# Kernel optimization log

Measured on AMD Instinct MI355X. Metric: run time of the kernel, lower is better.

Reference implementation:

```python
import jax, jax.numpy as jnp
import numpy as np

# graph sizes: G graphs of N_PER nodes each (block-diagonal batched graph)
G, N_PER, F, NHID, E_PER = 128, 512, 128, 128, 4096
N = G * N_PER
E = G * E_PER
L1, L2, L3 = 4, 2, 2            # PANConv filter sizes (conv1 uses init filter_size=4)
K1, K2, K3 = N_PER // 2, N_PER // 4, N_PER // 8  # ratio=0.5 top-k per pooling stage


def setup_inputs() -> dict:
    ks = jax.random.split(jax.random.key(0), 10)
    rng = np.random.default_rng(0)
    off = (np.arange(G) * N_PER)[:, None]
    src = (rng.integers(0, N_PER, size=(G, E_PER)) + off).reshape(-1)
    dst = (rng.integers(0, N_PER, size=(G, E_PER)) + off).reshape(-1)
    edge_index = jnp.asarray(np.stack([src, dst]).astype(np.int32))
    batch = jnp.repeat(jnp.arange(G, dtype=jnp.int32), N_PER)
    def w(k, shp, fan):
        return jax.random.normal(k, shp, jnp.float32) / np.float32(np.sqrt(fan))
    z = lambda *s: jnp.zeros(s, jnp.float32)
    return dict(
        x=jax.random.normal(ks[0], (N, F), jnp.float32),
        edge_index=edge_index, batch=batch,
        lump_W=w(ks[1], (F, NHID), F), lump_b=z(NHID),
        conv1_W=w(ks[2], (NHID, NHID), NHID), conv1_b=z(NHID),
        conv2_W=w(ks[3], (NHID, NHID), NHID), conv2_b=z(NHID),
        conv3_W=w(ks[4], (NHID, NHID), NHID), conv3_b=z(NHID),
        pool1_p=w(ks[5], (NHID,), NHID), pool1_beta=jnp.full((2,), 0.5, jnp.float32),
        pool2_p=w(ks[6], (NHID,), NHID), pool2_beta=jnp.full((2,), 0.5, jnp.float32),
        pool3_p=w(ks[7], (NHID,), NHID), pool3_beta=jnp.full((2,), 0.5, jnp.float32),
        lin1_W=w(ks[8], (NHID, NHID // 2), NHID), lin1_b=z(NHID // 2),
        lin2_W=w(ks[9], (NHID // 2, 1), NHID // 2), lin2_b=z(1),
    )


def _pan_prop(h, src, dst, ew, L):
    # (sum_{l=0..L} A^l) @ h, A weighted by edge weights ew, via iterated gather/scatter
    acc, y = h, h
    n = h.shape[0]
    for _ in range(L):
        y = jax.ops.segment_sum(y[src] * ew[:, None], dst, num_segments=n)
        acc = acc + y
    return acc


def _pan_conv(x, src, dst, ew, W, b, L):
    # PANConv: M = Z^{-1/2} (sum_{l<=L} A^l) Z^{-1/2};  out = M x W + b
    d = _pan_prop(jnp.ones((x.shape[0], 1), x.dtype), src, dst, ew, L)[:, 0]
    dinv = jax.lax.rsqrt(jnp.maximum(d, 1e-12))
    h = dinv[:, None] * _pan_prop(dinv[:, None] * x, src, dst, ew, L)
    return h @ W + b


def _pan_pool(x, src, dst, ew, p, beta, n_per, k):
    # PANPooling: score = beta0*(x.p)/||p|| + beta1*node_strength; per-graph top-k
    n = x.shape[0]
    deg = jax.ops.segment_sum(ew, dst, num_segments=n)
    score = beta[0] * (x @ p) / jnp.linalg.norm(p) + beta[1] * deg
    _, idx = jax.lax.top_k(score.reshape(G, n_per), k)          # [G, k] local indices
    perm = (idx + (jnp.arange(G) * n_per)[:, None]).reshape(-1)  # [G*k] global
    x_new = x[perm] * jnp.tanh(score[perm])[:, None]
    inv = jnp.zeros((n,), jnp.int32).at[perm].set(jnp.arange(G * k, dtype=jnp.int32))
    mask = jnp.zeros((n,), x.dtype).at[perm].set(1.0)
    # keep edge arrays fixed-size: dropped edges get weight 0 (same math as filtering)
    return x_new, inv[src], inv[dst], ew * mask[src] * mask[dst], perm


def reference(x, edge_index, batch, lump_W, lump_b, conv1_W, conv1_b, conv2_W, conv2_b,
              conv3_W, conv3_b, pool1_p, pool1_beta, pool2_p, pool2_beta, pool3_p,
              pool3_beta, lin1_W, lin1_b, lin2_W, lin2_b):
    src, dst = edge_index[0], edge_index[1]
    ew = jnp.ones((src.shape[0],), x.dtype)
    h = x @ lump_W + lump_b                                   # PANLump lift
    h = _pan_conv(h, src, dst, ew, conv1_W, conv1_b, L1)
    h, src, dst, ew, perm1 = _pan_pool(h, src, dst, ew, pool1_p, pool1_beta, N_PER, K1)
    h = _pan_conv(h, src, dst, ew, conv2_W, conv2_b, L2)
    h, src, dst, ew, perm2 = _pan_pool(h, src, dst, ew, pool2_p, pool2_beta, K1, K2)
    h = _pan_conv(h, src, dst, ew, conv3_W, conv3_b, L3)
    h, src, dst, ew, perm3 = _pan_pool(h, src, dst, ew, pool3_p, pool3_beta, K2, K3)
    seg = jnp.repeat(jnp.arange(G, dtype=jnp.int32), K3)
    mean = jax.ops.segment_sum(h, seg, num_segments=G) / jnp.float32(K3)  # scatter_mean
    out = jax.nn.relu(mean @ lin1_W + lin1_b) @ lin2_W + lin2_b           # [G, 1]
    return out
```

## Files before the change

### kernel.cpp

```cpp
#include <hip/hip_runtime.h>
#include <math.h>

#define G_     128
#define E_     524288
#define EPG    4096
#define DEGMAX 48

typedef __attribute__((ext_vector_type(8))) short bf16x8;
typedef __attribute__((ext_vector_type(4))) float f32x4;
typedef __attribute__((ext_vector_type(4))) unsigned short u16x4;

__device__ inline void split_bf16(float x, short& hi, short& lo){
    unsigned u = __float_as_uint(x);
    hi = (short)(u >> 16);
    float hf = __uint_as_float(u & 0xffff0000u);
    unsigned r = __float_as_uint(x - hf);
    lo = (short)(r >> 16);
}

__global__ __launch_bounds__(512) void k_prep1(const int* __restrict__ ei,
        int* __restrict__ cnt, unsigned short* __restrict__ csrcp,
        int* __restrict__ permg, float* __restrict__ dinvg){
    __shared__ int   lcnt[512];
    __shared__ float y[1024];
    __shared__ int   bins[64];
    __shared__ int   permS[512];
    int g = blockIdx.x, t = threadIdx.x, gbase = g*512;
    lcnt[t] = 0;
    if (t < 64) bins[t] = 0;
    __syncthreads();
    for (int i = t; i < EPG; i += 512){
        int e = g*EPG + i;
        int sv = ei[e] & 511;
        int d  = ei[E_ + e] & 511;
        int slot = atomicAdd(&lcnt[d], 1);
        if (slot < DEGMAX) csrcp[(size_t)(gbase + d)*DEGMAX + slot] = (unsigned short)sv;
    }
    __syncthreads();
    int rawc = lcnt[t];
    cnt[gbase + t] = rawc;
    int dc = min(rawc, DEGMAX);
    atomicAdd(&bins[dc], 1);
    __syncthreads();
    if (t < 64){
        int v0 = bins[t], s = v0;
        #pragma unroll
        for (int off = 1; off < 64; off <<= 1){
            int n = __shfl_up(s, off);
            if (t >= off) s += n;
        }
        bins[t] = s - v0;
    }
    __syncthreads();
    {
        int slot = atomicAdd(&bins[dc], 1);
        int pk = t | (dc << 16);
        permS[slot] = pk;
        permg[gbase + slot] = pk;
    }
    __syncthreads();
    int pk = permS[t];
    int pv = pk & 0xffff, pd = pk >> 16;
    y[pv] = 1.f;
    __syncthreads();
    float dacc = 1.f;
    int cur = 0;
    for (int l = 0; l < 4; l++){
        const float* la = &y[cur*512];
        float s = 0.f;
        int nq = (pd + 3) >> 2;
        const u16x4* cp = (const u16x4*)(csrcp + (size_t)(gbase + pv)*DEGMAX);
        u16x4 oc = cp[0];
        #pragma unroll 1
        for (int jq = 0; jq < nq; jq++){
            u16x4 ocn = cp[jq + 1];
            s += (la[(int)oc[0]] + la[(int)oc[1]]) + (la[(int)oc[2]] + la[(int)oc[3]]);
            oc = ocn;
        }
        if (nq) s -= (float)(nq*4 - pd) * la[0];
        y[(1^cur)*512 + pv] = s;
        dacc += s;
        __syncthreads();
        cur ^= 1;
    }
    dinvg[gbase + pv] = rsqrtf(fmaxf(dacc, 1e-12f));
}

template<int NPER, int L, int IT>
__global__ __launch_bounds__(1024)
void k_prop(const int* __restrict__ permg, const float* __restrict__ dinvg,
        const unsigned short* __restrict__ csrcp,
        const float* __restrict__ X, float* __restrict__ OUT){
    __shared__ __align__(16) float y[NPER*32];
    __shared__ float dinvs[NPER];
    int g = blockIdx.x, fq = blockIdx.y, gbase = g*NPER;
    int t = threadIdx.x;
    int f4 = (t & 7)*4;
    int fo = fq*32 + f4;
    if (t < NPER) dinvs[t] = dinvg[gbase + t];
    int pkr[IT];
    {
        int wv = t >> 6, gi = (t >> 3) & 7;
        #pragma unroll
        for (int it = 0; it < IT; it++){
            int ch = (it & 1) ? (15 - wv) : wv;
            pkr[it] = permg[gbase + (16*it + ch)*8 + gi];
        }
    }
    __syncthreads();
    float4 acc[IT];
    #pragma unroll
    for (int it = 0; it < IT; it++){
        int v = pkr[it] & 0xffff;
        float d = dinvs[v];
        float4 w = *(const float4*)&X[(size_t)(gbase + v)*128 + fo];
        w.x*=d; w.y*=d; w.z*=d; w.w*=d;
        acc[it] = w;
        *(float4*)&y[v*32 + f4] = w;
    }
    __syncthreads();
    for (int l = 0; l < L; l++){
        float4 s[IT];
        #pragma unroll
        for (int it = 0; it < IT; it++){
            int pk = pkr[it];
            int c = pk >> 16;
            int nq = (c + 3) >> 2;
            const u16x4* cp = (const u16x4*)(csrcp + (size_t)(gbase + (pk & 0xffff))*DEGMAX);
            float4 ss = make_float4(0.f,0.f,0.f,0.f);
            u16x4 oc = cp[0];
            #pragma unroll 1
            for (int jq = 0; jq < nq; jq++){
                u16x4 ocn = cp[jq + 1];
                float4 w0 = *(const float4*)&y[((int)oc[0])*32 + f4];
                float4 w1 = *(const float4*)&y[((int)oc[1])*32 + f4];
                float4 w2 = *(const float4*)&y[((int)oc[2])*32 + f4];
                float4 w3 = *(const float4*)&y[((int)oc[3])*32 + f4];
                ss.x += (w0.x + w1.x) + (w2.x + w3.x);
                ss.y += (w0.y + w1.y) + (w2.y + w3.y);
                ss.z += (w0.z + w1.z) + (w2.z + w3.z);
                ss.w += (w0.w + w1.w) + (w2.w + w3.w);
                oc = ocn;
            }
            if (nq){
                float fp = (float)(nq*4 - c);
                float4 z = *(const float4*)&y[f4];
                ss.x -= fp*z.x; ss.y -= fp*z.y; ss.z -= fp*z.z; ss.w -= fp*z.w;
            }
            s[it] = ss;
        }
        __syncthreads();
        #pragma unroll
        for (int it = 0; it < IT; it++){
            int v = pkr[it] & 0xffff;
            *(float4*)&y[v*32 + f4] = s[it];
            acc[it].x+=s[it].x; acc[it].y+=s[it].y; acc[it].z+=s[it].z; acc[it].w+=s[it].w;
        }
        __syncthreads();
    }
    #pragma unroll
    for (int it = 0; it < IT; it++){
        int v = pkr[it] & 0xffff;
        float d = dinvs[v];
        float4 w = acc[it];
        w.x*=d; w.y*=d; w.z*=d; w.w*=d;
        *(float4*)&OUT[(size_t)(gbase + v)*128 + fo] = w;
    }
}

template<int RT>
__global__ __launch_bounds__(256) void k_gemm_mfma(const float* __restrict__ X,
        const float* __restrict__ W, const float* __restrict__ bias, float* __restrict__ Y){
    __shared__ short wsh[128*136];
    __shared__ short wsl[128*136];
    __shared__ float bsh[128];
    int t = threadIdx.x;
    for (int e = t; e < 16384; e += 256){
        int k = e >> 7, n = e & 127;
        short hi, lo; split_bf16(W[e], hi, lo);
        wsh[n*136 + k] = hi; wsl[n*136 + k] = lo;
    }
    if (t < 128) bsh[t] = bias[t];
    __syncthreads();
    int wave = t >> 6, lane = t & 63;
    int ln = lane & 15, q = lane >> 4;
    size_t rb0 = (size_t)blockIdx.x * (64*RT);
    for (int rt = 0; rt < RT; rt++){
        size_t rb = rb0 + (size_t)rt*64;
        const float* xrow = &X[(rb + wave*16 + ln)*128 + q*8];
        f32x4 acc[8];
        #pragma unroll
        for (int i = 0; i < 8; i++) acc[i] = (f32x4){0.f,0.f,0.f,0.f};
        #pragma unroll
        for (int kc = 0; kc < 4; kc++){
            float4 xa = *(const float4*)(xrow + kc*32);
            float4 xb = *(const float4*)(xrow + kc*32 + 4);
            bf16x8 ah, al; short hi, lo;
            split_bf16(xa.x, hi, lo); ah[0]=hi; al[0]=lo;
            split_bf16(xa.y, hi, lo); ah[1]=hi; al[1]=lo;
            split_bf16(xa.z, hi, lo); ah[2]=hi; al[2]=lo;
            split_bf16(xa.w, hi, lo); ah[3]=hi; al[3]=lo;
            split_bf16(xb.x, hi, lo); ah[4]=hi; al[4]=lo;
            split_bf16(xb.y, hi, lo); ah[5]=hi; al[5]=lo;
            split_bf16(xb.z, hi, lo); ah[6]=hi; al[6]=lo;
            split_bf16(xb.w, hi, lo); ah[7]=hi; al[7]=lo;
            #pragma unroll
            for (int nt = 0; nt < 8; nt++){
                int wo = (nt*16 + ln)*136 + kc*32 + q*8;
                bf16x8 bh = *(const bf16x8*)&wsh[wo];
                bf16x8 bl = *(const bf16x8*)&wsl[wo];
                acc[nt] = __builtin_amdgcn_mfma_f32_16x16x32_bf16(ah, bh, acc[nt], 0, 0, 0);
                acc[nt] = __builtin_amdgcn_mfma_f32_16x16x32_bf16(ah, bl, acc[nt], 0, 0, 0);
                acc[nt] = __builtin_amdgcn_mfma_f32_16x16x32_bf16(al, bh, acc[nt], 0, 0, 0);
            }
        }
        #pragma unroll
        for (int nt = 0; nt < 8; nt++){
            int c = nt*16 + ln;
            float bb = bsh[c];
            #pragma unroll
            for (int r = 0; r < 4; r++){
                Y[(rb + wave*16 + q*4 + r)*128 + c] = acc[nt][r] + bb;
            }
        }
    }
}

template<int NPER, bool BUILD>
__global__ __launch_bounds__(512) void k_pooltop(const float* __restrict__ h, const float* __restrict__ p,
        const float* __restrict__ beta, const int* __restrict__ cnt,
        const int* __restrict__ esrc_in, const int* __restrict__ edst_in,
        int* __restrict__ esrc_out, int* __restrict__ edst_out,
        int* __restrict__ cnt_next, unsigned short* __restrict__ csrcp,
        int* __restrict__ permg, float* __restrict__ dinvg,
        float* __restrict__ hout){
    __shared__ __align__(16) float q[128];
    __shared__ __align__(16) float sc[NPER];
    __shared__ float th[NPER];
    __shared__ int  nid[NPER];
    __shared__ float red[64];
    __shared__ int  lcnt[NPER/2];
    __shared__ int  bins[64];
    __shared__ int  permS[NPER/2];
    const int K = NPER/2;
    int g = blockIdx.x, t = threadIdx.x, gbase = g*NPER;
    float b0 = beta[0], b1 = beta[1];
    if (BUILD && t < K) lcnt[t] = 0;
    if (t < 64) bins[t] = 0;
    if (t < 64){ float a = p[t], b = p[t+64]; red[t] = a*a + b*b; }
    __syncthreads();
    if (t == 0){ float s = 0.f; for (int i = 0; i < 64; i++) s += red[i]; red[0] = sqrtf(s); }
    __syncthreads();
    if (t < 128) q[t] = b0 * p[t] / red[0];
    __syncthreads();
    if (t < NPER){
        const float4* hr = (const float4*)(h + (size_t)(gbase + t)*128);
        const float4* q4 = (const float4*)q;
        float s = 0.f;
        #pragma unroll 8
        for (int j = 0; j < 32; j++){
            float4 a = hr[j], b = q4[j];
            s += a.x*b.x + a.y*b.y + a.z*b.z + a.w*b.w;
        }
        s += b1 * (float)cnt[gbase + t];
        sc[t] = s;
    }
    __syncthreads();
    if (t < NPER){
        float s = sc[t];
        int rank = 0;
        const float4* sc4 = (const float4*)sc;
        #pragma unroll 8
        for (int j4 = 0; j4 < NPER/4; j4++){
            float4 v = sc4[j4];
            int j = j4*4;
            rank += (v.x > s) || (v.x == s && (j+0) < t);
            rank += (v.y > s) || (v.y == s && (j+1) < t);
            rank += (v.z > s) || (v.z == s && (j+2) < t);
            rank += (v.w > s) || (v.w == s && (j+3) < t);
        }
        nid[t] = (rank < K) ? (g*K + rank) : -1;
        th[t] = tanhf(s);
    }
    __syncthreads();
    for (int base = t; base < NPER*32; base += 512){
        int v = base >> 5, f4 = base & 31;
        int ni = nid[v];
        if (ni >= 0){
            float tt = th[v];
            float4 w = *(const float4*)&h[(size_t)(gbase + v)*128 + f4*4];
            w.x*=tt; w.y*=tt; w.z*=tt; w.w*=tt;
            *(float4*)&hout[(size_t)ni*128 + f4*4] = w;
        }
    }
    if (BUILD){
        for (int i = t; i < EPG; i += 512){
            int e = g*EPG + i;
            int d = edst_in[e];
            if (d < 0) continue;
            int s_ = esrc_in[e];
            int ns = nid[s_ - gbase], nd = nid[d - gbase];
            if ((ns | nd) < 0){ edst_out[e] = -1; }
            else {
                esrc_out[e] = ns; edst_out[e] = nd;
                int slot = atomicAdd(&lcnt[nd & (K-1)], 1);
                if (slot < DEGMAX) csrcp[(size_t)nd*DEGMAX + slot] = (unsigned short)(ns & (K-1));
            }
        }
        __syncthreads();
        float* yd = sc;
        int rawc = 0, dc = 0;
        if (t < K){
            rawc = lcnt[t];
            cnt_next[g*K + t] = rawc;
            dc = min(rawc, DEGMAX);
            atomicAdd(&bins[dc], 1);
        }
        __syncthreads();
        if (t < 64){
            int v0 = bins[t], s = v0;
            #pragma unroll
            for (int off = 1; off < 64; off <<= 1){
                int n = __shfl_up(s, off);
                if (t >= off) s += n;
            }
            bins[t] = s - v0;
        }
        __syncthreads();
        if (t < K){
            int slot = atomicAdd(&bins[dc], 1);
            permS[slot] = t | (dc << 16);
            permg[g*K + slot] = permS[slot];
        }
        __syncthreads();
        int pv = 0, pd = 0;
        if (t < K){
            int pk = permS[t];
            pv = pk & 0xffff; pd = pk >> 16;
            yd[pv] = 1.f;
        }
        __syncthreads();
        float dacc = 1.f;
        int cur = 0;
        for (int l = 0; l < 2; l++){
            if (t < K){
                const float* la = &yd[cur*K];
                float s = 0.f;
                int nq = (pd + 3) >> 2;
                const u16x4* cp = (const u16x4*)(csrcp + (size_t)(g*K + pv)*DEGMAX);
                u16x4 oc = cp[0];
                #pragma unroll 1
                for (int jq = 0; jq < nq; jq++){
                    u16x4 ocn = cp[jq + 1];
                    s += (la[(int)oc[0]] + la[(int)oc[1]]) + (la[(int)oc[2]] + la[(int)oc[3]]);
                    oc = ocn;
                }
                if (nq) s -= (float)(nq*4 - pd) * la[0];
                yd[(1^cur)*K + pv] = s;
                dacc += s;
            }
            __syncthreads();
            cur ^= 1;
        }
        if (t < K) dinvg[g*K + pv] = rsqrtf(fmaxf(dacc, 1e-12f));
    }
}

__global__ __launch_bounds__(128) void k_meanmlp(const float* __restrict__ h, const float* __restrict__ W1,
        const float* __restrict__ b1, const float* __restrict__ W2, const float* __restrict__ b2,
        float* __restrict__ out){
    __shared__ float mr[128];
    int g = blockIdx.x, t = threadIdx.x;
    float s = 0.f;
    #pragma unroll 8
    for (int r = 0; r < 64; r++) s += h[((size_t)g*64 + r)*128 + t];
    mr[t] = s * (1.f/64.f);
    __syncthreads();
    if (t < 64){
        float a = b1[t];
        #pragma unroll 8
        for (int k = 0; k < 128; k++) a += mr[k]*W1[k*64 + t];
        a = fmaxf(a, 0.f);
        float r = a * W2[t];
        #pragma unroll
        for (int off = 32; off > 0; off >>= 1) r += __shfl_down(r, off);
        if (t == 0) out[g] = r + b2[0];
    }
}

extern "C" void kernel_launch(void* const* d_in, const int* in_sizes, int n_in,
                              void* d_out, int out_size, void* d_ws, size_t ws_size,
                              hipStream_t stream){
    (void)in_sizes; (void)n_in; (void)out_size; (void)ws_size;
    const float* x     = (const float*)d_in[0];
    const int*   ei    = (const int*)d_in[1];
    const float* lumpW = (const float*)d_in[3];
    const float* lumpb = (const float*)d_in[4];
    const float* convW[3]    = {(const float*)d_in[5], (const float*)d_in[7], (const float*)d_in[9]};
    const float* convB[3]    = {(const float*)d_in[6], (const float*)d_in[8], (const float*)d_in[10]};
    const float* poolP[3]    = {(const float*)d_in[11], (const float*)d_in[13], (const float*)d_in[15]};
    const float* poolBeta[3] = {(const float*)d_in[12], (const float*)d_in[14], (const float*)d_in[16]};
    const float* lin1W = (const float*)d_in[17];
    const float* lin1b = (const float*)d_in[18];
    const float* lin2W = (const float*)d_in[19];
    const float* lin2b = (const float*)d_in[20];
    float* out = (float*)d_out;

    char* w8 = (char*)d_ws;
    size_t off = 0;
    auto alloc = [&](size_t bytes)->char*{
        char* p = w8 + off; off += (bytes + 255) & ~(size_t)255; return p;
    };
    float* A     = (float*)alloc((size_t)65536*128*4);
    float* Bb    = (float*)alloc((size_t)65536*128*4);
    float* Cc    = (float*)alloc((size_t)32768*128*4);
    int*   srcA  = (int*)alloc((size_t)E_*4);
    int*   dstA  = (int*)alloc((size_t)E_*4);
    unsigned short* csr1 = (unsigned short*)alloc((size_t)65536*DEGMAX*2);
    unsigned short* csr2 = (unsigned short*)alloc((size_t)32768*DEGMAX*2);
    unsigned short* csr3 = (unsigned short*)alloc((size_t)16384*DEGMAX*2);
    int*   cntA  = (int*)alloc((size_t)(65536+32768+16384)*4);
    int*   cnt1 = cntA, *cnt2 = cntA + 65536, *cnt3 = cntA + 98304;
    int*   perm1 = (int*)alloc((size_t)65536*4);
    int*   perm2 = (int*)alloc((size_t)32768*4);
    int*   perm3 = (int*)alloc((size_t)16384*4);
    float* dinv1 = (float*)alloc((size_t)65536*4);
    float* dinv2 = (float*)alloc((size_t)32768*4);
    float* dinv3 = (float*)alloc((size_t)16384*4);

    dim3 b256(256);

    size_t zbytes = (size_t)(65536+32768+16384)*DEGMAX*2;
    hipMemsetAsync(csr1, 0, zbytes, stream);
    k_gemm_mfma<2><<<512, b256, 0, stream>>>(x, lumpW, lumpb, A);
    k_prep1<<<G_, 512, 0, stream>>>(ei, cnt1, csr1, perm1, dinv1);

    k_prop<512,4,4><<<dim3(G_,4), 1024, 0, stream>>>(perm1, dinv1, csr1, A, Bb);
    k_gemm_mfma<2><<<512, b256, 0, stream>>>(Bb, convW[0], convB[0], A);
    k_pooltop<512,true><<<G_, 512, 0, stream>>>(A, poolP[0], poolBeta[0], cnt1,
            ei, ei + E_, srcA, dstA, cnt2, csr2, perm2, dinv2, Cc);

    k_prop<256,2,2><<<dim3(G_,4), 1024, 0, stream>>>(perm2, dinv2, csr2, Cc, Bb);
    k_gemm_mfma<1><<<512, b256, 0, stream>>>(Bb, convW[1], convB[1], A);
    k_pooltop<256,true><<<G_, 512, 0, stream>>>(A, poolP[1], poolBeta[1], cnt2,
            srcA, dstA, srcA, dstA, cnt3, csr3, perm3, dinv3, Cc);

    k_prop<128,2,1><<<dim3(G_,4), 1024, 0, stream>>>(perm3, dinv3, csr3, Cc, Bb);
    k_gemm_mfma<1><<<256, b256, 0, stream>>>(Bb, convW[2], convB[2], A);
    k_pooltop<128,false><<<G_, 512, 0, stream>>>(A, poolP[2], poolBeta[2], cnt3,
            nullptr, nullptr, nullptr, nullptr, nullptr, nullptr, nullptr, nullptr, Cc);

    k_meanmlp<<<G_, 128, 0, stream>>>(Cc, lin1W, lin1b, lin2W, lin2b, out);
}
```

Baseline: 341.6 us.

## Fuse pool score into GEMM epilogue and gather selected rows lazily

Computes the pooling score (projection onto normalized p plus beta1 times degree) inside the GEMM epilogue, using shuffle reductions over the accumulator tiles. The top-k kernel no longer reads the full feature matrix or writes a compacted, tanh-scaled copy. It emits selected row indices and tanh factors instead, and the next propagation and mean-MLP kernels gather rows through those indices and apply the scale. This removes a full read and write of the feature matrix per pooling stage, at the cost of indirect row gathers in the consumers.

```diff
diff --git a/kernel.cpp b/kernel.cpp
--- a/kernel.cpp
+++ b/kernel.cpp
@@ -86,11 +86,12 @@
     dinvg[gbase + pv] = rsqrtf(fmaxf(dacc, 1e-12f));
 }
 
-template<int NPER, int L, int IT>
+template<int NPER, int L, int IT, bool SEL>
 __global__ __launch_bounds__(1024)
 void k_prop(const int* __restrict__ permg, const float* __restrict__ dinvg,
         const unsigned short* __restrict__ csrcp,
-        const float* __restrict__ X, float* __restrict__ OUT){
+        const float* __restrict__ X, const int* __restrict__ selg,
+        const float* __restrict__ thg, float* __restrict__ OUT){
     __shared__ __align__(16) float y[NPER*32];
     __shared__ float dinvs[NPER];
     int g = blockIdx.x, fq = blockIdx.y, gbase = g*NPER;
@@ -113,7 +114,14 @@
     for (int it = 0; it < IT; it++){
         int v = pkr[it] & 0xffff;
         float d = dinvs[v];
-        float4 w = *(const float4*)&X[(size_t)(gbase + v)*128 + fo];
+        size_t row;
+        if (SEL){
+            row = (size_t)selg[gbase + v];
+            d *= thg[gbase + v];
+        } else {
+            row = (size_t)(gbase + v);
+        }
+        float4 w = *(const float4*)&X[row*128 + fo];
         w.x*=d; w.y*=d; w.z*=d; w.w*=d;
         acc[it] = w;
         *(float4*)&y[v*32 + f4] = w;
@@ -170,10 +178,14 @@
 
 template<int RT>
 __global__ __launch_bounds__(256) void k_gemm_mfma(const float* __restrict__ X,
-        const float* __restrict__ W, const float* __restrict__ bias, float* __restrict__ Y){
+        const float* __restrict__ W, const float* __restrict__ bias, float* __restrict__ Y,
+        const float* __restrict__ p, const float* __restrict__ beta,
+        const int* __restrict__ cntv, float* __restrict__ score){
     __shared__ short wsh[128*136];
     __shared__ short wsl[128*136];
     __shared__ float bsh[128];
+    __shared__ float qs[128];
+    __shared__ float rednorm[64];
     int t = threadIdx.x;
     for (int e = t; e < 16384; e += 256){
         int k = e >> 7, n = e & 127;
@@ -181,7 +193,16 @@
         wsh[n*136 + k] = hi; wsl[n*136 + k] = lo;
     }
     if (t < 128) bsh[t] = bias[t];
-    __syncthreads();
+    if (score && t < 64){ float a = p[t], b = p[t+64]; rednorm[t] = a*a + b*b; }
+    __syncthreads();
+    float b1 = 0.f;
+    if (score){
+        if (t == 0){ float s = 0.f; for (int i = 0; i < 64; i++) s += rednorm[i]; rednorm[0] = sqrtf(s); }
+        __syncthreads();
+        if (t < 128) qs[t] = beta[0] * p[t] / rednorm[0];
+        b1 = beta[1];
+        __syncthreads();
+    }
     int wave = t >> 6, lane = t & 63;
     int ln = lane & 15, q = lane >> 4;
     size_t rb0 = (size_t)blockIdx.x * (64*RT);
@@ -223,48 +244,45 @@
                 Y[(rb + wave*16 + q*4 + r)*128 + c] = acc[nt][r] + bb;
             }
         }
+        if (score){
+            #pragma unroll
+            for (int r = 0; r < 4; r++){
+                float sp = 0.f;
+                #pragma unroll
+                for (int nt = 0; nt < 8; nt++){
+                    int c = nt*16 + ln;
+                    sp += (acc[nt][r] + bsh[c]) * qs[c];
+                }
+                sp += __shfl_xor(sp, 1);
+                sp += __shfl_xor(sp, 2);
+                sp += __shfl_xor(sp, 4);
+                sp += __shfl_xor(sp, 8);
+                if (ln == 0){
+                    int row = (int)rb + wave*16 + q*4 + r;
+                    score[row] = sp + b1 * (float)cntv[row];
+                }
+            }
+        }
     }
 }
 
 template<int NPER, bool BUILD>
-__global__ __launch_bounds__(512) void k_pooltop(const float* __restrict__ h, const float* __restrict__ p,
-        const float* __restrict__ beta, const int* __restrict__ cnt,
+__global__ __launch_bounds__(512) void k_pooltop(const float* __restrict__ score_in,
         const int* __restrict__ esrc_in, const int* __restrict__ edst_in,
         int* __restrict__ esrc_out, int* __restrict__ edst_out,
         int* __restrict__ cnt_next, unsigned short* __restrict__ csrcp,
         int* __restrict__ permg, float* __restrict__ dinvg,
-        float* __restrict__ hout){
-    __shared__ __align__(16) float q[128];
+        int* __restrict__ selg, float* __restrict__ thg){
     __shared__ __align__(16) float sc[NPER];
-    __shared__ float th[NPER];
     __shared__ int  nid[NPER];
-    __shared__ float red[64];
     __shared__ int  lcnt[NPER/2];
     __shared__ int  bins[64];
     __shared__ int  permS[NPER/2];
     const int K = NPER/2;
     int g = blockIdx.x, t = threadIdx.x, gbase = g*NPER;
-    float b0 = beta[0], b1 = beta[1];
     if (BUILD && t < K) lcnt[t] = 0;
     if (t < 64) bins[t] = 0;
-    if (t < 64){ float a = p[t], b = p[t+64]; red[t] = a*a + b*b; }
-    __syncthreads();
-    if (t == 0){ float s = 0.f; for (int i = 0; i < 64; i++) s += red[i]; red[0] = sqrtf(s); }
-    __syncthreads();
-    if (t < 128) q[t] = b0 * p[t] / red[0];
-    __syncthreads();
-    if (t < NPER){
-        const float4* hr = (const float4*)(h + (size_t)(gbase + t)*128);
-        const float4* q4 = (const float4*)q;
-        float s = 0.f;
-        #pragma unroll 8
-        for (int j = 0; j < 32; j++){
-            float4 a = hr[j], b = q4[j];
-            s += a.x*b.x + a.y*b.y + a.z*b.z + a.w*b.w;
-        }
-        s += b1 * (float)cnt[gbase + t];
-        sc[t] = s;
-    }
+    if (t < NPER) sc[t] = score_in[gbase + t];
     __syncthreads();
     if (t < NPER){
         float s = sc[t];
@@ -279,20 +297,13 @@
             rank += (v.z > s) || (v.z == s && (j+2) < t);
             rank += (v.w > s) || (v.w == s && (j+3) < t);
         }
-        nid[t] = (rank < K) ? (g*K + rank) : -1;
-        th[t] = tanhf(s);
-    }
-    __syncthreads();
-    for (int base = t; base < NPER*32; base += 512){
-        int v = base >> 5, f4 = base & 31;
-        int ni = nid[v];
-        if (ni >= 0){
-            float tt = th[v];
-            float4 w = *(const float4*)&h[(size_t)(gbase + v)*128 + f4*4];
-            w.x*=tt; w.y*=tt; w.z*=tt; w.w*=tt;
-            *(float4*)&hout[(size_t)ni*128 + f4*4] = w;
-        }
-    }
+        if (rank < K){
+            nid[t] = g*K + rank;
+            selg[g*K + rank] = gbase + t;
+            thg[g*K + rank]  = tanhf(s);
+        } else nid[t] = -1;
+    }
+    __syncthreads();
     if (BUILD){
         for (int i = t; i < EPG; i += 512){
             int e = g*EPG + i;
@@ -366,14 +377,19 @@
     }
 }
 
-__global__ __launch_bounds__(128) void k_meanmlp(const float* __restrict__ h, const float* __restrict__ W1,
-        const float* __restrict__ b1, const float* __restrict__ W2, const float* __restrict__ b2,
+__global__ __launch_bounds__(128) void k_meanmlp(const float* __restrict__ h,
+        const int* __restrict__ selg, const float* __restrict__ thg,
+        const float* __restrict__ W1, const float* __restrict__ b1,
+        const float* __restrict__ W2, const float* __restrict__ b2,
         float* __restrict__ out){
     __shared__ float mr[128];
     int g = blockIdx.x, t = threadIdx.x;
     float s = 0.f;
     #pragma unroll 8
-    for (int r = 0; r < 64; r++) s += h[((size_t)g*64 + r)*128 + t];
+    for (int r = 0; r < 64; r++){
+        int row = selg[g*64 + r];
+        s += h[(size_t)row*128 + t] * thg[g*64 + r];
+    }
     mr[t] = s * (1.f/64.f);
     __syncthreads();
     if (t < 64){
@@ -413,7 +429,6 @@
     };
     float* A     = (float*)alloc((size_t)65536*128*4);
     float* Bb    = (float*)alloc((size_t)65536*128*4);
-    float* Cc    = (float*)alloc((size_t)32768*128*4);
     int*   srcA  = (int*)alloc((size_t)E_*4);
     int*   dstA  = (int*)alloc((size_t)E_*4);
     unsigned short* csr1 = (unsigned short*)alloc((size_t)65536*DEGMAX*2);
@@ -427,28 +442,44 @@
     float* dinv1 = (float*)alloc((size_t)65536*4);
     float* dinv2 = (float*)alloc((size_t)32768*4);
     float* dinv3 = (float*)alloc((size_t)16384*4);
+    float* score1 = (float*)alloc((size_t)65536*4);
+    float* score2 = (float*)alloc((size_t)32768*4);
+    float* score3 = (float*)alloc((size_t)16384*4);
+    int*   sel2  = (int*)alloc((size_t)32768*4);
+    int*   sel3  = (int*)alloc((size_t)16384*4);
+    int*   sel4  = (int*)alloc((size_t)8192*4);
+    float* th2   = (float*)alloc((size_t)32768*4);
+    float* th3   = (float*)alloc((size_t)16384*4);
+    float* th4   = (float*)alloc((size_t)8192*4);
 
     dim3 b256(256);
 
     size_t zbytes = (size_t)(65536+32768+16384)*DEGMAX*2;
     hipMemsetAsync(csr1, 0, zbytes, stream);
-    k_gemm_mfma<2><<<512, b256, 0, stream>>>(x, lumpW, lumpb, A);
+    k_gemm_mfma<2><<<512, b256, 0, stream>>>(x, lumpW, lumpb, A,
+            nullptr, nullptr, nullptr, nullptr);
     k_prep1<<<G_, 512, 0, stream>>>(ei, cnt1, csr1, perm1, dinv1);
 
-    k_prop<512,4,4><<<dim3(G_,4), 1024, 0, stream>>>(perm1, dinv1, csr1, A, Bb);
-    k_gemm_mfma<2><<<512, b256, 0, stream>>>(Bb, convW[0], convB[0], A);
-    k_pooltop<512,true><<<G_, 512, 0, stream>>>(A, poolP[0], poolBeta[0], cnt1,
-            ei, ei + E_, srcA, dstA, cnt2, csr2, perm2, dinv2, Cc);
-
-    k_prop<256,2,2><<<dim3(G_,4), 1024, 0, stream>>>(perm2, dinv2, csr2, Cc, Bb);
-    k_gemm_mfma<1><<<512, b256, 0, stream>>>(Bb, convW[1], convB[1], A);
-    k_pooltop<256,true><<<G_, 512, 0, stream>>>(A, poolP[1], poolBeta[1], cnt2,
-            srcA, dstA, srcA, dstA, cnt3, csr3, perm3, dinv3, Cc);
-
-    k_prop<128,2,1><<<dim3(G_,4), 1024, 0, stream>>>(perm3, dinv3, csr3, Cc, Bb);
-    k_gemm_mfma<1><<<256, b256, 0, stream>>>(Bb, convW[2], convB[2], A);
-    k_pooltop<128,false><<<G_, 512, 0, stream>>>(A, poolP[2], poolBeta[2], cnt3,
-            nullptr, nullptr, nullptr, nullptr, nullptr, nullptr, nullptr, nullptr, Cc);
-
-    k_meanmlp<<<G_, 128, 0, stream>>>(Cc, lin1W, lin1b, lin2W, lin2b, out);
-}
+    k_prop<512,4,4,false><<<dim3(G_,4), 1024, 0, stream>>>(perm1, dinv1, csr1, A,
+            nullptr, nullptr, Bb);
+    k_gemm_mfma<2><<<512, b256, 0, stream>>>(Bb, convW[0], convB[0], A,
+            poolP[0], poolBeta[0], cnt1, score1);
+    k_pooltop<512,true><<<G_, 512, 0, stream>>>(score1, ei, ei + E_, srcA, dstA,
+            cnt2, csr2, perm2, dinv2, sel2, th2);
+
+    k_prop<256,2,2,true><<<dim3(G_,4), 1024, 0, stream>>>(perm2, dinv2, csr2, A,
+            sel2, th2, Bb);
+    k_gemm_mfma<1><<<512, b256, 0, stream>>>(Bb, convW[1], convB[1], A,
+            poolP[1], poolBeta[1], cnt2, score2);
+    k_pooltop<256,true><<<G_, 512, 0, stream>>>(score2, srcA, dstA, srcA, dstA,
+            cnt3, csr3, perm3, dinv3, sel3, th3);
+
+    k_prop<128,2,1,true><<<dim3(G_,4), 1024, 0, stream>>>(perm3, dinv3, csr3, A,
+            sel3, th3, Bb);
+    k_gemm_mfma<1><<<256, b256, 0, stream>>>(Bb, convW[2], convB[2], A,
+            poolP[2], poolBeta[2], cnt3, score3);
+    k_pooltop<128,false><<<G_, 512, 0, stream>>>(score3, nullptr, nullptr, nullptr, nullptr,
+            nullptr, nullptr, nullptr, nullptr, sel4, th4);
+
+    k_meanmlp<<<G_, 128, 0, stream>>>(A, sel4, th4, lin1W, lin1b, lin2W, lin2b, out);
+}
```

New measurement: 309.1 us. -9.5%, faster.
